# Kernel tuning notes

Measured on AMD Instinct MI355X. Metric: run time of the kernel, lower is better.

Reference implementation:

```python
import jax, jax.numpy as jnp
import numpy as np

B, S, D = 64, 256, 512          # batch, seq_len_max, num_dim (= in_dim = nclass)
H, DO = 8, 64                   # num_heads, out_dim per head (H*DO == D)
ALPHA = 0.2                     # leaky_relu negative slope
N = B * S                       # nodes
DEG = 32
E = N * DEG + N                 # random edges + self-loops


def setup_inputs() -> dict:
    key = jax.random.key(0)
    k = jax.random.split(key, 7)
    h = jax.random.normal(k[0], (B, S, D), jnp.float32)
    loops = jnp.arange(N, dtype=jnp.int32)
    src = jnp.concatenate([jax.random.randint(k[1], (N * DEG,), 0, N, jnp.int32), loops])
    dst = jnp.concatenate([jax.random.randint(k[2], (N * DEG,), 0, N, jnp.int32), loops])
    W1 = jax.random.normal(k[3], (H, D, DO), jnp.float32) * 0.05      # per-head fc weight
    a1 = jax.random.normal(k[4], (H, 2 * DO), jnp.float32) * 0.05     # per-head attn_fc weight
    Wout = jax.random.normal(k[5], (H * DO, D), jnp.float32) * 0.05   # out_att fc
    aout = jax.random.normal(k[6], (2 * D,), jnp.float32) * 0.05      # out_att attn_fc
    return {"h": h, "W1": W1, "a1": a1, "Wout": Wout, "aout": aout, "src": src, "dst": dst}


def gat_head(x, W, a, src, dst, concat):
    # x: [N, in_d], W: [in_d, d], a: [2d]
    z = x @ W                                   # [N, d]
    d = W.shape[1]
    es = z @ a[:d]                              # src part of attn score, [N]
    ed = z @ a[d:]                              # dst part, [N]
    e = jax.nn.leaky_relu(es[src] + ed[dst], ALPHA)   # [E]
    # segment softmax over incoming edges of each dst node
    m = jax.ops.segment_max(e, dst, num_segments=N)
    m = jnp.where(jnp.isfinite(m), m, 0.0)
    ex = jnp.exp(e - m[dst])
    den = jax.ops.segment_sum(ex, dst, num_segments=N)
    att = ex / den[dst]                         # [E] (self-loops guarantee den > 0)
    out = jax.ops.segment_sum(att[:, None] * z[src], dst, num_segments=N)  # [N, d]
    return jax.nn.elu(out) if concat else out


def reference(h, W1, a1, Wout, aout, src, dst):
    x = h.reshape(N, D)                         # dropout is identity at eval
    heads = jax.vmap(lambda W, a: gat_head(x, W, a, src, dst, True))(W1, a1)  # [H, N, DO]
    hcat = jnp.transpose(heads, (1, 0, 2)).reshape(N, H * DO)                 # [N, H*DO]
    out = jax.nn.elu(gat_head(hcat, Wout, aout, src, dst, False))             # [N, D]
    return (out + x).reshape(B, S, D)
```

## Files before the change

### kernel.cpp

```cpp
#include <hip/hip_runtime.h>
#include <stdint.h>

#define DD 512
#define HH 8
#define DOO 64
#define ALPHA 0.2f

typedef __attribute__((ext_vector_type(8))) short short8;
typedef __attribute__((ext_vector_type(4))) float floatx4;
typedef __attribute__((ext_vector_type(4))) unsigned short u16x4;
typedef unsigned short u16;

static __device__ __forceinline__ float bf2f(u16 u){
  union { unsigned int u; float f; } c; c.u = ((unsigned int)u) << 16; return c.f;
}
static __device__ __forceinline__ u16 f2bf(float f){
  union { float f; unsigned int u; } c; c.f = f;
  unsigned int u = c.u;
  unsigned int r = (u + 0x7FFFu + ((u >> 16) & 1u)) >> 16;
  return (u16)r;
}
static __device__ __forceinline__ float leaky(float s){ return (s >= 0.f) ? s : ALPHA * s; }
static __device__ __forceinline__ float elu(float v){ return (v > 0.f) ? v : (__expf(v) - 1.f); }

#define PERM_LO 0x01000504u
#define PERM_HI 0x03020706u

#define DOT2(accv, pairv, wv) \
  asm("v_dot2_f32_bf16 %0, %1, %2, %0" : "+v"(accv) : "v"(pairv), "v"(wv))

#define GLOAD_LDS16(g, l) \
  __builtin_amdgcn_global_load_lds((const __attribute__((address_space(1))) void*)(g), \
                                   (__attribute__((address_space(3))) void*)(l), 16, 0, 0)

__global__ void k_prep(const float* __restrict__ h, u16* __restrict__ xb,
                       const float* __restrict__ W1, u16* __restrict__ wbt1,
                       const float* __restrict__ Wout, u16* __restrict__ wbt2,
                       const int* __restrict__ dst, int* deg,
                       int n4, int E){
  int i = blockIdx.x * blockDim.x + threadIdx.x;
  if (i < n4){
    float4 v = ((const float4*)h)[i];
    u16x4 o;
    o[0] = f2bf(v.x); o[1] = f2bf(v.y); o[2] = f2bf(v.z); o[3] = f2bf(v.w);
    ((u16x4*)xb)[i] = o;
    return;
  }
  i -= n4;
  if (i < HH * DD * DOO / 8){
    int idx0 = i * 8;
    #pragma unroll
    for (int t = 0; t < 8; t++){
      int idx = idx0 + t;
      int hh = idx >> 15;
      int rem = idx & 32767;
      int k = rem >> 6;
      int dd = rem & 63;
      wbt1[(hh * 64 + dd) * DD + k] = f2bf(W1[idx]);
    }
    return;
  }
  i -= HH * DD * DOO / 8;
  if (i < DD * DD){
    int k = i >> 9, n = i & 511;
    wbt2[n * DD + k] = f2bf(Wout[i]);
    return;
  }
  i -= DD * DD;
  if (i < E) atomicAdd(&deg[dst[i]], 1);
}

__global__ void k_scan(const int* __restrict__ deg, int* __restrict__ off, int N){
  __shared__ int sm[1024];
  int tid = threadIdx.x;
  const int per = 16;
  int base = tid * per;
  int loc[per];
  int t = 0;
  #pragma unroll
  for (int i = 0; i < per; i++){
    int v = (base + i < N) ? deg[base + i] : 0;
    v = (v + 3) & ~3;
    loc[i] = v; t += v;
  }
  sm[tid] = t; __syncthreads();
  for (int o = 1; o < 1024; o <<= 1){
    int v = 0;
    if (tid >= o) v = sm[tid - o];
    __syncthreads();
    sm[tid] += v;
    __syncthreads();
  }
  int run = sm[tid] - t;
  #pragma unroll
  for (int i = 0; i < per; i++){ if (base + i < N) off[base + i] = run; run += loc[i]; }
  if (tid == 1023) off[N] = run;
}

__global__ void k_scatter(const int* __restrict__ src, const int* __restrict__ dst,
                          const int* __restrict__ off, int* cursor, int* __restrict__ csr,
                          int E, int N){
  int i = blockIdx.x * blockDim.x + threadIdx.x;
  if (i < 256){
    csr[off[N] + i] = 0;
  }
  if (i < E){
    int d = dst[i];
    int p = atomicAdd(&cursor[d], 1);
    csr[off[d] + p] = src[i];
  }
}

__global__ __launch_bounds__(256) void k_gemm(const u16* __restrict__ A,
                                              const u16* __restrict__ BT,
                                              u16* __restrict__ C, int M){
  __shared__ __attribute__((aligned(16))) u16 As[128 * 64];
  __shared__ __attribute__((aligned(16))) u16 Bs[128 * 64];
  const int tid = threadIdx.x;
  const int wid = tid >> 6, lane = tid & 63;
  const int n0 = blockIdx.x * 128, m0 = blockIdx.y * 128;
  const int wr = wid >> 1, wc = wid & 1;
  const int row16 = lane & 15, kg = lane >> 4;
  floatx4 acc[4][4];
  #pragma unroll
  for (int i = 0; i < 4; i++)
    #pragma unroll
    for (int j = 0; j < 4; j++) acc[i][j] = (floatx4)0.0f;

  for (int kt = 0; kt < DD; kt += 64){
    #pragma unroll
    for (int i = 0; i < 4; i++){
      int chunk = i * 256 + tid;
      int m = chunk >> 3, g = chunk & 7;
      int gs = g ^ (m & 7);
      GLOAD_LDS16(A + (size_t)(m0 + m) * DD + kt + gs * 8, &As[chunk * 8]);
      GLOAD_LDS16(BT + (size_t)(n0 + m) * DD + kt + gs * 8, &Bs[chunk * 8]);
    }
    __syncthreads();
    short8 af[4][2], bf[4][2];
    #pragma unroll
    for (int mi = 0; mi < 4; mi++)
      #pragma unroll
      for (int kk = 0; kk < 2; kk++){
        int row = wr * 64 + mi * 16 + row16;
        int gr = (kk * 4 + kg) ^ (row & 7);
        af[mi][kk] = *(const short8*)(&As[(row * 8 + gr) * 8]);
      }
    #pragma unroll
    for (int ni = 0; ni < 4; ni++)
      #pragma unroll
      for (int kk = 0; kk < 2; kk++){
        int row = wc * 64 + ni * 16 + row16;
        int gr = (kk * 4 + kg) ^ (row & 7);
        bf[ni][kk] = *(const short8*)(&Bs[(row * 8 + gr) * 8]);
      }
    #pragma unroll
    for (int kk = 0; kk < 2; kk++)
      #pragma unroll
      for (int mi = 0; mi < 4; mi++)
        #pragma unroll
        for (int ni = 0; ni < 4; ni++)
          acc[mi][ni] = __builtin_amdgcn_mfma_f32_16x16x32_bf16(af[mi][kk], bf[ni][kk], acc[mi][ni], 0, 0, 0);
    __syncthreads();
  }
  #pragma unroll
  for (int mi = 0; mi < 4; mi++)
    #pragma unroll
    for (int ni = 0; ni < 4; ni++)
      #pragma unroll
      for (int j = 0; j < 4; j++){
        int r = m0 + wr * 64 + mi * 16 + kg * 4 + j;
        int c = n0 + wc * 64 + ni * 16 + row16;
        C[(size_t)r * DD + c] = f2bf(acc[mi][ni][j]);
      }
}

__global__ void k_scores1(const u16* __restrict__ z, const float* __restrict__ a1,
                          float* __restrict__ es, float* __restrict__ ed, int N){
  int wid = threadIdx.x >> 6, lane = threadIdx.x & 63;
  int n = blockIdx.x * 4 + wid;
  if (n >= N) return;
  int h = lane >> 3, j8 = lane & 7;
  short8 zv = *(const short8*)(z + (size_t)n * DD + lane * 8);
  float esv = 0.f, edv = 0.f;
  #pragma unroll
  for (int t = 0; t < 8; t++){
    float f = bf2f((u16)zv[t]);
    esv += f * a1[h * 128 + j8 * 8 + t];
    edv += f * a1[h * 128 + 64 + j8 * 8 + t];
  }
  #pragma unroll
  for (int d2 = 1; d2 < 8; d2 <<= 1){ esv += __shfl_xor(esv, d2); edv += __shfl_xor(edv, d2); }
  if (j8 == 0){ es[n * 8 + h] = esv; ed[n * 8 + h] = edv; }
}

__global__ void k_scores2(const u16* __restrict__ z, const float* __restrict__ aout,
                          float* __restrict__ es, float* __restrict__ ed, int N){
  int wid = threadIdx.x >> 6, lane = threadIdx.x & 63;
  int n = blockIdx.x * 4 + wid;
  if (n >= N) return;
  short8 zv = *(const short8*)(z + (size_t)n * DD + lane * 8);
  float esv = 0.f, edv = 0.f;
  #pragma unroll
  for (int t = 0; t < 8; t++){
    float f = bf2f((u16)zv[t]);
    esv += f * aout[lane * 8 + t];
    edv += f * aout[512 + lane * 8 + t];
  }
  #pragma unroll
  for (int d2 = 1; d2 < 64; d2 <<= 1){ esv += __shfl_xor(esv, d2); edv += __shfl_xor(edv, d2); }
  if (lane == 0){ es[n] = esv; ed[n] = edv; }
}

__global__ void k_edgew1(const float* __restrict__ es, const float* __restrict__ ed,
                         const int* __restrict__ off, const int* __restrict__ deg,
                         int* __restrict__ csr, unsigned* __restrict__ wp,
                         float* __restrict__ den1, int N, int ep2){
  int wid = threadIdx.x >> 6, lane = threadIdx.x & 63;
  int n = blockIdx.x * 4 + wid;
  if (n >= N) return;
  int o0 = off[n], cntp = off[n + 1] - o0, cnt = deg[n];
  float edh[8];
  {
    float4 d0 = *(const float4*)(ed + (size_t)n * 8);
    float4 d1 = *(const float4*)(ed + (size_t)n * 8 + 4);
    edh[0]=d0.x; edh[1]=d0.y; edh[2]=d0.z; edh[3]=d0.w;
    edh[4]=d1.x; edh[5]=d1.y; edh[6]=d1.z; edh[7]=d1.w;
  }
  float den[8];
  #pragma unroll
  for (int h = 0; h < 8; h++) den[h] = 0.f;
  for (int base = 0; base < cntp; base += 64){
    int e = base + lane;
    float wv[8];
    if (e < cnt){
      int s = csr[o0 + e];
      float4 e0 = *(const float4*)(es + (size_t)s * 8);
      float4 e1 = *(const float4*)(es + (size_t)s * 8 + 4);
      float ev[8] = {e0.x, e0.y, e0.z, e0.w, e1.x, e1.y, e1.z, e1.w};
      #pragma unroll
      for (int h = 0; h < 8; h++){
        float w = __expf(leaky(ev[h] + edh[h]));
        wv[h] = w; den[h] += w;
      }
    } else {
      if (e < cntp) csr[o0 + e] = 0;
      #pragma unroll
      for (int h = 0; h < 8; h++) wv[h] = 0.f;
    }
    #pragma unroll
    for (int h = 0; h < 8; h++){
      float wn = __shfl_down(wv[h], 1);
      if (!(lane & 1) && e < cntp){
        unsigned pk;
        asm("v_cvt_pk_bf16_f32 %0, %1, %2" : "=v"(pk) : "v"(wv[h]), "v"(wn));
        wp[(size_t)h * ep2 + ((o0 + e) >> 1)] = pk;
      }
    }
  }
  #pragma unroll
  for (int h = 0; h < 8; h++){
    float d = den[h];
    #pragma unroll
    for (int d2 = 1; d2 < 64; d2 <<= 1) d += __shfl_xor(d, d2);
    if (lane == 0) den1[(size_t)n * 8 + h] = d;
  }
}

__global__ void k_edgew2(const float* __restrict__ es, const float* __restrict__ ed,
                         const int* __restrict__ off, const int* __restrict__ deg,
                         int* __restrict__ csr, unsigned* __restrict__ wp,
                         float* __restrict__ den2, int N){
  int wid = threadIdx.x >> 6, lane = threadIdx.x & 63;
  int n = blockIdx.x * 4 + wid;
  if (n >= N) return;
  int o0 = off[n], cntp = off[n + 1] - o0, cnt = deg[n];
  float edn = ed[n];
  float dsum = 0.f;
  for (int base = 0; base < cntp; base += 64){
    int e = base + lane;
    float w = 0.f;
    if (e < cnt){
      int s = csr[o0 + e];
      w = __expf(leaky(es[s] + edn));
      dsum += w;
    } else if (e < cntp){
      csr[o0 + e] = 0;
    }
    float wn = __shfl_down(w, 1);
    if (!(lane & 1) && e < cntp){
      unsigned pk;
      asm("v_cvt_pk_bf16_f32 %0, %1, %2" : "=v"(pk) : "v"(w), "v"(wn));
      wp[(o0 + e) >> 1] = pk;
    }
  }
  #pragma unroll
  for (int d2 = 1; d2 < 64; d2 <<= 1) dsum += __shfl_xor(dsum, d2);
  if (lane == 0) den2[n] = dsum;
}

__global__ __launch_bounds__(256) void k_agg1(const u16* __restrict__ z,
    const unsigned* __restrict__ wp, const float* __restrict__ den1,
    const int* __restrict__ off, const int* __restrict__ csr,
    u16* __restrict__ hcat, int N, int ep2){
  int wid = __builtin_amdgcn_readfirstlane(threadIdx.x >> 6);
  int lane = threadIdx.x & 63;
  int n = blockIdx.x * 4 + wid;
  if (n >= N) return;
  int p = blockIdx.y;
  int o0 = off[n];
  int itn = (off[n + 1] - o0) >> 2;
  const int4* cp4 = (const int4*)(csr + o0);
  const unsigned* zd = (const unsigned*)z + (size_t)p * 64 + lane;
  int head = 2 * p + (lane >> 5);
  const unsigned* wpb = wp + (size_t)head * ep2 + (o0 >> 1);
  float acc0 = 0.f, acc1 = 0.f;

  int4 c0 = cp4[0], c1 = cp4[1];
  uint2 a0 = *(const uint2*)(wpb);
  uint2 a1 = *(const uint2*)(wpb + 2);
  unsigned dA0 = zd[(size_t)(unsigned)c0.x * 256], dA1 = zd[(size_t)(unsigned)c0.y * 256];
  unsigned dB0 = zd[(size_t)(unsigned)c0.z * 256], dB1 = zd[(size_t)(unsigned)c0.w * 256];
  unsigned eA0 = zd[(size_t)(unsigned)c1.x * 256], eA1 = zd[(size_t)(unsigned)c1.y * 256];
  unsigned eB0 = zd[(size_t)(unsigned)c1.z * 256], eB1 = zd[(size_t)(unsigned)c1.w * 256];

  for (int it = 0; it < itn; ++it){
    int4 cn = cp4[it + 2];
    uint2 an = *(const uint2*)(wpb + 2 * it + 4);
    unsigned nA0 = zd[(size_t)(unsigned)cn.x * 256], nA1 = zd[(size_t)(unsigned)cn.y * 256];
    unsigned nB0 = zd[(size_t)(unsigned)cn.z * 256], nB1 = zd[(size_t)(unsigned)cn.w * 256];
    unsigned pr;
    pr = __builtin_amdgcn_perm(dA0, dA1, PERM_LO); DOT2(acc0, pr, a0.x);
    pr = __builtin_amdgcn_perm(dA0, dA1, PERM_HI); DOT2(acc1, pr, a0.x);
    pr = __builtin_amdgcn_perm(dB0, dB1, PERM_LO); DOT2(acc0, pr, a0.y);
    pr = __builtin_amdgcn_perm(dB0, dB1, PERM_HI); DOT2(acc1, pr, a0.y);
    dA0 = eA0; dA1 = eA1; dB0 = eB0; dB1 = eB1; a0 = a1;
    eA0 = nA0; eA1 = nA1; eB0 = nB0; eB1 = nB1; a1 = an;
  }
  float inv = 1.f / den1[(size_t)n * 8 + head];
  unsigned od = (unsigned)f2bf(elu(acc0 * inv)) | ((unsigned)f2bf(elu(acc1 * inv)) << 16);
  ((unsigned*)(hcat + (size_t)n * DD))[p * 64 + lane] = od;
}

__global__ __launch_bounds__(256) void k_agg2(const u16* __restrict__ z,
    const unsigned* __restrict__ wp, const float* __restrict__ den2,
    const int* __restrict__ off, const int* __restrict__ csr,
    const u16* __restrict__ xb, float* __restrict__ out, int N){
  int wid = __builtin_amdgcn_readfirstlane(threadIdx.x >> 6);
  int lane = threadIdx.x & 63;
  int n = blockIdx.x * 4 + wid;
  if (n >= N) return;
  int p = blockIdx.y;
  int o0 = off[n];
  int itn = (off[n + 1] - o0) >> 2;
  const int4* cp4 = (const int4*)(csr + o0);
  const unsigned* zd = (const unsigned*)z + (size_t)p * 64 + lane;
  const unsigned* wpb = wp + (o0 >> 1);
  float acc0 = 0.f, acc1 = 0.f;

  int4 c0 = cp4[0], c1 = cp4[1];
  uint2 a0 = *(const uint2*)(wpb);
  uint2 a1 = *(const uint2*)(wpb + 2);
  unsigned dA0 = zd[(size_t)(unsigned)c0.x * 256], dA1 = zd[(size_t)(unsigned)c0.y * 256];
  unsigned dB0 = zd[(size_t)(unsigned)c0.z * 256], dB1 = zd[(size_t)(unsigned)c0.w * 256];
  unsigned eA0 = zd[(size_t)(unsigned)c1.x * 256], eA1 = zd[(size_t)(unsigned)c1.y * 256];
  unsigned eB0 = zd[(size_t)(unsigned)c1.z * 256], eB1 = zd[(size_t)(unsigned)c1.w * 256];

  for (int it = 0; it < itn; ++it){
    int4 cn = cp4[it + 2];
    uint2 an = *(const uint2*)(wpb + 2 * it + 4);
    unsigned nA0 = zd[(size_t)(unsigned)cn.x * 256], nA1 = zd[(size_t)(unsigned)cn.y * 256];
    unsigned nB0 = zd[(size_t)(unsigned)cn.z * 256], nB1 = zd[(size_t)(unsigned)cn.w * 256];
    unsigned pr;
    pr = __builtin_amdgcn_perm(dA0, dA1, PERM_LO); DOT2(acc0, pr, a0.x);
    pr = __builtin_amdgcn_perm(dA0, dA1, PERM_HI); DOT2(acc1, pr, a0.x);
    pr = __builtin_amdgcn_perm(dB0, dB1, PERM_LO); DOT2(acc0, pr, a0.y);
    pr = __builtin_amdgcn_perm(dB0, dB1, PERM_HI); DOT2(acc1, pr, a0.y);
    dA0 = eA0; dA1 = eA1; dB0 = eB0; dB1 = eB1; a0 = a1;
    eA0 = nA0; eA1 = nA1; eB0 = nB0; eB1 = nB1; a1 = an;
  }
  float inv = 1.f / den2[n];
  unsigned xv = ((const unsigned*)(xb + (size_t)n * DD))[p * 64 + lane];
  float2 o2;
  o2.x = elu(acc0 * inv) + bf2f((u16)(xv & 0xFFFFu));
  o2.y = elu(acc1 * inv) + bf2f((u16)(xv >> 16));
  *(float2*)(out + (size_t)n * DD + p * 128 + lane * 2) = o2;
}

extern "C" void kernel_launch(void* const* d_in, const int* in_sizes, int n_in,
                              void* d_out, int out_size, void* d_ws, size_t ws_size,
                              hipStream_t stream){
  const float* h   = (const float*)d_in[0];
  const float* W1  = (const float*)d_in[1];
  const float* a1  = (const float*)d_in[2];
  const float* Wout= (const float*)d_in[3];
  const float* aout= (const float*)d_in[4];
  const int* src   = (const int*)d_in[5];
  const int* dst   = (const int*)d_in[6];
  float* out = (float*)d_out;
  const int N = in_sizes[0] / DD;
  const int E = in_sizes[5];
  const int EP = E + 3 * N + 512;
  const int ep2 = EP >> 1;

  char* p = (char*)d_ws;
  auto alloc = [&](size_t bytes) -> char* {
    char* r = p;
    p += (bytes + 255) & ~(size_t)255;
    return r;
  };
  u16* xb    = (u16*)alloc((size_t)N * DD * 2);
  u16* z1b   = (u16*)alloc((size_t)N * DD * 2);
  u16* hcat  = (u16*)alloc((size_t)N * DD * 2);
  u16* wbt1  = (u16*)alloc((size_t)DD * DD * 2);
  u16* wbt2  = (u16*)alloc((size_t)DD * DD * 2);
  float* es1 = (float*)alloc((size_t)N * HH * 4);
  float* ed1 = (float*)alloc((size_t)N * HH * 4);
  float* es2 = (float*)alloc((size_t)N * 4);
  float* ed2 = (float*)alloc((size_t)N * 4);
  float* den1= (float*)alloc((size_t)N * HH * 4);
  float* den2= (float*)alloc((size_t)N * 4);
  int* deg   = (int*)alloc((size_t)N * 4);
  int* off   = (int*)alloc((size_t)(N + 1) * 4);
  int* cursor= (int*)alloc((size_t)N * 4);
  int* csr   = (int*)alloc((size_t)EP * 4);
  unsigned* wp1 = (unsigned*)alloc(((size_t)HH * ep2 + 64) * 4);
  unsigned* wp2 = (unsigned*)alloc(((size_t)ep2 + 64) * 4);

  hipMemsetAsync(deg, 0, (size_t)((char*)csr - (char*)deg), stream);

  int n4 = N * DD / 4;
  int prep_threads = n4 + HH * DD * DOO / 8 + DD * DD + E;
  k_prep<<<(prep_threads + 255) / 256, 256, 0, stream>>>(h, xb, W1, wbt1, Wout, wbt2, dst, deg, n4, E);
  k_scan<<<1, 1024, 0, stream>>>(deg, off, N);
  k_scatter<<<(E + 255) / 256, 256, 0, stream>>>(src, dst, off, cursor, csr, E, N);

  dim3 gg(DD / 128, N / 128);
  dim3 ga((N + 3) / 4, 4);
  dim3 gw((N + 3) / 4);

  k_gemm<<<gg, 256, 0, stream>>>(xb, wbt1, z1b, N);
  k_scores1<<<(N + 3) / 4, 256, 0, stream>>>(z1b, a1, es1, ed1, N);
  k_edgew1<<<gw, 256, 0, stream>>>(es1, ed1, off, deg, csr, wp1, den1, N, ep2);
  k_agg1<<<ga, 256, 0, stream>>>(z1b, wp1, den1, off, csr, hcat, N, ep2);

  k_gemm<<<gg, 256, 0, stream>>>(hcat, wbt2, z1b, N);
  k_scores2<<<(N + 3) / 4, 256, 0, stream>>>(z1b, aout, es2, ed2, N);
  k_edgew2<<<gw, 256, 0, stream>>>(es2, ed2, off, deg, csr, wp2, den2, N);
  k_agg2<<<ga, 256, 0, stream>>>(z1b, wp2, den2, off, csr, xb, out, N);
}
```

Before: 252.3 us.

## Remap aggregation to one column per lane with sentinel-padded CSR

The aggregation kernels now map each lane to a single 16-bit column of one 64-wide slice, using 8 slices per node instead of 4 slices with two columns per lane. This removes the per-edge perm work but doubles the number of blocks and gathers only 2 bytes per lane per edge. CSR padding now uses a sentinel index N that points to a zeroed extra row of z, and the cursor is initialised to the offsets, so the edge-weight kernels read csr without branching and no longer write to it. This adds the k_ntot and k_fillpad launches.

```diff
diff --git a/kernel.cpp b/kernel.cpp
--- a/kernel.cpp
+++ b/kernel.cpp
@@ -23,11 +23,11 @@
 static __device__ __forceinline__ float leaky(float s){ return (s >= 0.f) ? s : ALPHA * s; }
 static __device__ __forceinline__ float elu(float v){ return (v > 0.f) ? v : (__expf(v) - 1.f); }
 
-#define PERM_LO 0x01000504u
-#define PERM_HI 0x03020706u
-
 #define DOT2(accv, pairv, wv) \
   asm("v_dot2_f32_bf16 %0, %1, %2, %0" : "+v"(accv) : "v"(pairv), "v"(wv))
+
+#define PACK2(dst, lo, hi) \
+  asm("v_lshl_or_b32 %0, %1, 16, %2" : "=v"(dst) : "v"(hi), "v"(lo))
 
 #define GLOAD_LDS16(g, l) \
   __builtin_amdgcn_global_load_lds((const __attribute__((address_space(1))) void*)(g), \
@@ -36,8 +36,8 @@
 __global__ void k_prep(const float* __restrict__ h, u16* __restrict__ xb,
                        const float* __restrict__ W1, u16* __restrict__ wbt1,
                        const float* __restrict__ Wout, u16* __restrict__ wbt2,
-                       const int* __restrict__ dst, int* deg,
-                       int n4, int E){
+                       const int* __restrict__ dst, int* deg, u16* __restrict__ z1b,
+                       int n4, int E, int N){
   int i = blockIdx.x * blockDim.x + threadIdx.x;
   if (i < n4){
     float4 v = ((const float4*)h)[i];
@@ -67,10 +67,24 @@
     return;
   }
   i -= DD * DD;
-  if (i < E) atomicAdd(&deg[dst[i]], 1);
-}
-
-__global__ void k_scan(const int* __restrict__ deg, int* __restrict__ off, int N){
+  if (i < E){
+    atomicAdd(&deg[dst[i]], 1);
+    return;
+  }
+  i -= E;
+  if (i < DD / 4){
+    u16x4 zz; zz[0]=0; zz[1]=0; zz[2]=0; zz[3]=0;
+    ((u16x4*)(z1b + (size_t)N * DD))[i] = zz;
+  }
+}
+
+__global__ void k_ntot(const int* __restrict__ deg, int* __restrict__ ntot, int N){
+  int n = blockIdx.x * blockDim.x + threadIdx.x;
+  if (n < N) ntot[n] = (deg[n] + 3) & ~3;
+}
+
+__global__ void k_scan(const int* __restrict__ ntot, int* __restrict__ off,
+                       int* __restrict__ cursor, int N){
   __shared__ int sm[1024];
   int tid = threadIdx.x;
   const int per = 16;
@@ -78,11 +92,7 @@
   int loc[per];
   int t = 0;
   #pragma unroll
-  for (int i = 0; i < per; i++){
-    int v = (base + i < N) ? deg[base + i] : 0;
-    v = (v + 3) & ~3;
-    loc[i] = v; t += v;
-  }
+  for (int i = 0; i < per; i++){ int v = (base + i < N) ? ntot[base + i] : 0; loc[i] = v; t += v; }
   sm[tid] = t; __syncthreads();
   for (int o = 1; o < 1024; o <<= 1){
     int v = 0;
@@ -93,7 +103,10 @@
   }
   int run = sm[tid] - t;
   #pragma unroll
-  for (int i = 0; i < per; i++){ if (base + i < N) off[base + i] = run; run += loc[i]; }
+  for (int i = 0; i < per; i++){
+    if (base + i < N){ off[base + i] = run; cursor[base + i] = run; }
+    run += loc[i];
+  }
   if (tid == 1023) off[N] = run;
 }
 
@@ -101,14 +114,22 @@
                           const int* __restrict__ off, int* cursor, int* __restrict__ csr,
                           int E, int N){
   int i = blockIdx.x * blockDim.x + threadIdx.x;
-  if (i < 256){
-    csr[off[N] + i] = 0;
+  if (i < 512){
+    csr[off[N] + i] = N;
   }
   if (i < E){
     int d = dst[i];
     int p = atomicAdd(&cursor[d], 1);
-    csr[off[d] + p] = src[i];
-  }
+    csr[p] = src[i];
+  }
+}
+
+__global__ void k_fillpad(const int* __restrict__ off, const int* __restrict__ cursor,
+                          int* __restrict__ csr, int N){
+  int n = blockIdx.x * blockDim.x + threadIdx.x;
+  if (n >= N) return;
+  int e = off[n + 1];
+  for (int q = cursor[n]; q < e; q++) csr[q] = N;
 }
 
 __global__ __launch_bounds__(256) void k_gemm(const u16* __restrict__ A,
@@ -213,13 +234,13 @@
 }
 
 __global__ void k_edgew1(const float* __restrict__ es, const float* __restrict__ ed,
-                         const int* __restrict__ off, const int* __restrict__ deg,
-                         int* __restrict__ csr, unsigned* __restrict__ wp,
+                         const int* __restrict__ off,
+                         const int* __restrict__ csr, unsigned* __restrict__ wp,
                          float* __restrict__ den1, int N, int ep2){
   int wid = threadIdx.x >> 6, lane = threadIdx.x & 63;
   int n = blockIdx.x * 4 + wid;
   if (n >= N) return;
-  int o0 = off[n], cntp = off[n + 1] - o0, cnt = deg[n];
+  int o0 = off[n], cntp = off[n + 1] - o0;
   float edh[8];
   {
     float4 d0 = *(const float4*)(ed + (size_t)n * 8);
@@ -232,21 +253,17 @@
   for (int h = 0; h < 8; h++) den[h] = 0.f;
   for (int base = 0; base < cntp; base += 64){
     int e = base + lane;
+    int s = csr[o0 + e];
+    bool valid = (e < cntp) && (s != N);
+    float4 e0 = *(const float4*)(es + (size_t)s * 8);
+    float4 e1 = *(const float4*)(es + (size_t)s * 8 + 4);
+    float ev[8] = {e0.x, e0.y, e0.z, e0.w, e1.x, e1.y, e1.z, e1.w};
     float wv[8];
-    if (e < cnt){
-      int s = csr[o0 + e];
-      float4 e0 = *(const float4*)(es + (size_t)s * 8);
-      float4 e1 = *(const float4*)(es + (size_t)s * 8 + 4);
-      float ev[8] = {e0.x, e0.y, e0.z, e0.w, e1.x, e1.y, e1.z, e1.w};
-      #pragma unroll
-      for (int h = 0; h < 8; h++){
-        float w = __expf(leaky(ev[h] + edh[h]));
-        wv[h] = w; den[h] += w;
-      }
-    } else {
-      if (e < cntp) csr[o0 + e] = 0;
-      #pragma unroll
-      for (int h = 0; h < 8; h++) wv[h] = 0.f;
+    #pragma unroll
+    for (int h = 0; h < 8; h++){
+      float w = __expf(leaky(ev[h] + edh[h]));
+      wv[h] = valid ? w : 0.f;
+      den[h] += wv[h];
     }
     #pragma unroll
     for (int h = 0; h < 8; h++){
@@ -268,25 +285,22 @@
 }
 
 __global__ void k_edgew2(const float* __restrict__ es, const float* __restrict__ ed,
-                         const int* __restrict__ off, const int* __restrict__ deg,
-                         int* __restrict__ csr, unsigned* __restrict__ wp,
+                         const int* __restrict__ off,
+                         const int* __restrict__ csr, unsigned* __restrict__ wp,
                          float* __restrict__ den2, int N){
   int wid = threadIdx.x >> 6, lane = threadIdx.x & 63;
   int n = blockIdx.x * 4 + wid;
   if (n >= N) return;
-  int o0 = off[n], cntp = off[n + 1] - o0, cnt = deg[n];
+  int o0 = off[n], cntp = off[n + 1] - o0;
   float edn = ed[n];
   float dsum = 0.f;
   for (int base = 0; base < cntp; base += 64){
     int e = base + lane;
-    float w = 0.f;
-    if (e < cnt){
-      int s = csr[o0 + e];
-      w = __expf(leaky(es[s] + edn));
-      dsum += w;
-    } else if (e < cntp){
-      csr[o0 + e] = 0;
-    }
+    int s = csr[o0 + e];
+    bool valid = (e < cntp) && (s != N);
+    float w = __expf(leaky(es[s] + edn));
+    w = valid ? w : 0.f;
+    dsum += w;
     float wn = __shfl_down(w, 1);
     if (!(lane & 1) && e < cntp){
       unsigned pk;
@@ -303,88 +317,92 @@
     const unsigned* __restrict__ wp, const float* __restrict__ den1,
     const int* __restrict__ off, const int* __restrict__ csr,
     u16* __restrict__ hcat, int N, int ep2){
-  int wid = __builtin_amdgcn_readfirstlane(threadIdx.x >> 6);
-  int lane = threadIdx.x & 63;
-  int n = blockIdx.x * 4 + wid;
-  if (n >= N) return;
-  int p = blockIdx.y;
+  int tid = threadIdx.x;
+  int wid = tid >> 6, lane = tid & 63;
+  int s = blockIdx.x & 7;
+  int n = (blockIdx.x >> 3) * 4 + wid;
+  if (n >= N) return;
   int o0 = off[n];
   int itn = (off[n + 1] - o0) >> 2;
   const int4* cp4 = (const int4*)(csr + o0);
-  const unsigned* zd = (const unsigned*)z + (size_t)p * 64 + lane;
-  int head = 2 * p + (lane >> 5);
-  const unsigned* wpb = wp + (size_t)head * ep2 + (o0 >> 1);
-  float acc0 = 0.f, acc1 = 0.f;
-
-  int4 c0 = cp4[0], c1 = cp4[1];
-  uint2 a0 = *(const uint2*)(wpb);
-  uint2 a1 = *(const uint2*)(wpb + 2);
-  unsigned dA0 = zd[(size_t)(unsigned)c0.x * 256], dA1 = zd[(size_t)(unsigned)c0.y * 256];
-  unsigned dB0 = zd[(size_t)(unsigned)c0.z * 256], dB1 = zd[(size_t)(unsigned)c0.w * 256];
-  unsigned eA0 = zd[(size_t)(unsigned)c1.x * 256], eA1 = zd[(size_t)(unsigned)c1.y * 256];
-  unsigned eB0 = zd[(size_t)(unsigned)c1.z * 256], eB1 = zd[(size_t)(unsigned)c1.w * 256];
-
+  const uint2* wpb = (const uint2*)(wp + (size_t)s * ep2 + (o0 >> 1));
+  const u16* zs = z + s * 64 + lane;
+  float acc = 0.f;
+
+  unsigned dA0, dA1, dB0, dB1, eA0, eA1, eB0, eB1;
+  uint2 aq0, aq1;
+  int4 c1;
+  {
+    int4 c0 = cp4[0];
+    c1 = cp4[1];
+    aq0 = wpb[0]; aq1 = wpb[1];
+    dA0 = zs[(size_t)(unsigned)c0.x * DD]; dA1 = zs[(size_t)(unsigned)c0.y * DD];
+    dB0 = zs[(size_t)(unsigned)c0.z * DD]; dB1 = zs[(size_t)(unsigned)c0.w * DD];
+    eA0 = zs[(size_t)(unsigned)c1.x * DD]; eA1 = zs[(size_t)(unsigned)c1.y * DD];
+    eB0 = zs[(size_t)(unsigned)c1.z * DD]; eB1 = zs[(size_t)(unsigned)c1.w * DD];
+  }
   for (int it = 0; it < itn; ++it){
     int4 cn = cp4[it + 2];
-    uint2 an = *(const uint2*)(wpb + 2 * it + 4);
-    unsigned nA0 = zd[(size_t)(unsigned)cn.x * 256], nA1 = zd[(size_t)(unsigned)cn.y * 256];
-    unsigned nB0 = zd[(size_t)(unsigned)cn.z * 256], nB1 = zd[(size_t)(unsigned)cn.w * 256];
-    unsigned pr;
-    pr = __builtin_amdgcn_perm(dA0, dA1, PERM_LO); DOT2(acc0, pr, a0.x);
-    pr = __builtin_amdgcn_perm(dA0, dA1, PERM_HI); DOT2(acc1, pr, a0.x);
-    pr = __builtin_amdgcn_perm(dB0, dB1, PERM_LO); DOT2(acc0, pr, a0.y);
-    pr = __builtin_amdgcn_perm(dB0, dB1, PERM_HI); DOT2(acc1, pr, a0.y);
-    dA0 = eA0; dA1 = eA1; dB0 = eB0; dB1 = eB1; a0 = a1;
-    eA0 = nA0; eA1 = nA1; eB0 = nB0; eB1 = nB1; a1 = an;
-  }
-  float inv = 1.f / den1[(size_t)n * 8 + head];
-  unsigned od = (unsigned)f2bf(elu(acc0 * inv)) | ((unsigned)f2bf(elu(acc1 * inv)) << 16);
-  ((unsigned*)(hcat + (size_t)n * DD))[p * 64 + lane] = od;
+    uint2 an = wpb[it + 2];
+    unsigned nA0 = zs[(size_t)(unsigned)cn.x * DD], nA1 = zs[(size_t)(unsigned)cn.y * DD];
+    unsigned nB0 = zs[(size_t)(unsigned)cn.z * DD], nB1 = zs[(size_t)(unsigned)cn.w * DD];
+    unsigned pA, pB;
+    PACK2(pA, dA0, dA1);
+    PACK2(pB, dB0, dB1);
+    DOT2(acc, pA, aq0.x);
+    DOT2(acc, pB, aq0.y);
+    dA0 = eA0; dA1 = eA1; dB0 = eB0; dB1 = eB1; aq0 = aq1;
+    eA0 = nA0; eA1 = nA1; eB0 = nB0; eB1 = nB1; aq1 = an;
+  }
+  float inv = 1.f / den1[(size_t)n * 8 + s];
+  hcat[(size_t)n * DD + s * 64 + lane] = f2bf(elu(acc * inv));
 }
 
 __global__ __launch_bounds__(256) void k_agg2(const u16* __restrict__ z,
     const unsigned* __restrict__ wp, const float* __restrict__ den2,
     const int* __restrict__ off, const int* __restrict__ csr,
     const u16* __restrict__ xb, float* __restrict__ out, int N){
-  int wid = __builtin_amdgcn_readfirstlane(threadIdx.x >> 6);
-  int lane = threadIdx.x & 63;
-  int n = blockIdx.x * 4 + wid;
-  if (n >= N) return;
-  int p = blockIdx.y;
+  int tid = threadIdx.x;
+  int wid = tid >> 6, lane = tid & 63;
+  int s = blockIdx.x & 7;
+  int n = (blockIdx.x >> 3) * 4 + wid;
+  if (n >= N) return;
   int o0 = off[n];
   int itn = (off[n + 1] - o0) >> 2;
   const int4* cp4 = (const int4*)(csr + o0);
-  const unsigned* zd = (const unsigned*)z + (size_t)p * 64 + lane;
-  const unsigned* wpb = wp + (o0 >> 1);
-  float acc0 = 0.f, acc1 = 0.f;
-
-  int4 c0 = cp4[0], c1 = cp4[1];
-  uint2 a0 = *(const uint2*)(wpb);
-  uint2 a1 = *(const uint2*)(wpb + 2);
-  unsigned dA0 = zd[(size_t)(unsigned)c0.x * 256], dA1 = zd[(size_t)(unsigned)c0.y * 256];
-  unsigned dB0 = zd[(size_t)(unsigned)c0.z * 256], dB1 = zd[(size_t)(unsigned)c0.w * 256];
-  unsigned eA0 = zd[(size_t)(unsigned)c1.x * 256], eA1 = zd[(size_t)(unsigned)c1.y * 256];
-  unsigned eB0 = zd[(size_t)(unsigned)c1.z * 256], eB1 = zd[(size_t)(unsigned)c1.w * 256];
-
+  const uint2* wpb = (const uint2*)(wp + (o0 >> 1));
+  const u16* zs = z + s * 64 + lane;
+  float acc = 0.f;
+
+  unsigned dA0, dA1, dB0, dB1, eA0, eA1, eB0, eB1;
+  uint2 aq0, aq1;
+  int4 c1;
+  {
+    int4 c0 = cp4[0];
+    c1 = cp4[1];
+    aq0 = wpb[0]; aq1 = wpb[1];
+    dA0 = zs[(size_t)(unsigned)c0.x * DD]; dA1 = zs[(size_t)(unsigned)c0.y * DD];
+    dB0 = zs[(size_t)(unsigned)c0.z * DD]; dB1 = zs[(size_t)(unsigned)c0.w * DD];
+    eA0 = zs[(size_t)(unsigned)c1.x * DD]; eA1 = zs[(size_t)(unsigned)c1.y * DD];
+    eB0 = zs[(size_t)(unsigned)c1.z * DD]; eB1 = zs[(size_t)(unsigned)c1.w * DD];
+  }
   for (int it = 0; it < itn; ++it){
     int4 cn = cp4[it + 2];
-    uint2 an = *(const uint2*)(wpb + 2 * it + 4);
-    unsigned nA0 = zd[(size_t)(unsigned)cn.x * 256], nA1 = zd[(size_t)(unsigned)cn.y * 256];
-    unsigned nB0 = zd[(size_t)(unsigned)cn.z * 256], nB1 = zd[(size_t)(unsigned)cn.w * 256];
-    unsigned pr;
-    pr = __builtin_amdgcn_perm(dA0, dA1, PERM_LO); DOT2(acc0, pr, a0.x);
-    pr = __builtin_amdgcn_perm(dA0, dA1, PERM_HI); DOT2(acc1, pr, a0.x);
-    pr = __builtin_amdgcn_perm(dB0, dB1, PERM_LO); DOT2(acc0, pr, a0.y);
-    pr = __builtin_amdgcn_perm(dB0, dB1, PERM_HI); DOT2(acc1, pr, a0.y);
-    dA0 = eA0; dA1 = eA1; dB0 = eB0; dB1 = eB1; a0 = a1;
-    eA0 = nA0; eA1 = nA1; eB0 = nB0; eB1 = nB1; a1 = an;
+    uint2 an = wpb[it + 2];
+    unsigned nA0 = zs[(size_t)(unsigned)cn.x * DD], nA1 = zs[(size_t)(unsigned)cn.y * DD];
+    unsigned nB0 = zs[(size_t)(unsigned)cn.z * DD], nB1 = zs[(size_t)(unsigned)cn.w * DD];
+    unsigned pA, pB;
+    PACK2(pA, dA0, dA1);
+    PACK2(pB, dB0, dB1);
+    DOT2(acc, pA, aq0.x);
+    DOT2(acc, pB, aq0.y);
+    dA0 = eA0; dA1 = eA1; dB0 = eB0; dB1 = eB1; aq0 = aq1;
+    eA0 = nA0; eA1 = nA1; eB0 = nB0; eB1 = nB1; aq1 = an;
   }
   float inv = 1.f / den2[n];
-  unsigned xv = ((const unsigned*)(xb + (size_t)n * DD))[p * 64 + lane];
-  float2 o2;
-  o2.x = elu(acc0 * inv) + bf2f((u16)(xv & 0xFFFFu));
-  o2.y = elu(acc1 * inv) + bf2f((u16)(xv >> 16));
-  *(float2*)(out + (size_t)n * DD + p * 128 + lane * 2) = o2;
+  int c = s * 64 + lane;
+  float xv = bf2f(xb[(size_t)n * DD + c]);
+  out[(size_t)n * DD + c] = elu(acc * inv) + xv;
 }
 
 extern "C" void kernel_launch(void* const* d_in, const int* in_sizes, int n_in,
@@ -410,42 +428,46 @@
     return r;
   };
   u16* xb    = (u16*)alloc((size_t)N * DD * 2);
-  u16* z1b   = (u16*)alloc((size_t)N * DD * 2);
+  u16* z1b   = (u16*)alloc((size_t)(N + 1) * DD * 2);
   u16* hcat  = (u16*)alloc((size_t)N * DD * 2);
   u16* wbt1  = (u16*)alloc((size_t)DD * DD * 2);
   u16* wbt2  = (u16*)alloc((size_t)DD * DD * 2);
-  float* es1 = (float*)alloc((size_t)N * HH * 4);
+  float* es1 = (float*)alloc(((size_t)N * HH + 8) * 4);
   float* ed1 = (float*)alloc((size_t)N * HH * 4);
-  float* es2 = (float*)alloc((size_t)N * 4);
+  float* es2 = (float*)alloc(((size_t)N + 8) * 4);
   float* ed2 = (float*)alloc((size_t)N * 4);
   float* den1= (float*)alloc((size_t)N * HH * 4);
   float* den2= (float*)alloc((size_t)N * 4);
   int* deg   = (int*)alloc((size_t)N * 4);
+  int* ntot  = (int*)alloc((size_t)N * 4);
   int* off   = (int*)alloc((size_t)(N + 1) * 4);
   int* cursor= (int*)alloc((size_t)N * 4);
   int* csr   = (int*)alloc((size_t)EP * 4);
   unsigned* wp1 = (unsigned*)alloc(((size_t)HH * ep2 + 64) * 4);
   unsigned* wp2 = (unsigned*)alloc(((size_t)ep2 + 64) * 4);
 
-  hipMemsetAsync(deg, 0, (size_t)((char*)csr - (char*)deg), stream);
+  hipMemsetAsync(deg, 0, (size_t)N * 4, stream);
 
   int n4 = N * DD / 4;
-  int prep_threads = n4 + HH * DD * DOO / 8 + DD * DD + E;
-  k_prep<<<(prep_threads + 255) / 256, 256, 0, stream>>>(h, xb, W1, wbt1, Wout, wbt2, dst, deg, n4, E);
-  k_scan<<<1, 1024, 0, stream>>>(deg, off, N);
+  int prep_threads = n4 + HH * DD * DOO / 8 + DD * DD + E + DD / 4;
+  k_prep<<<(prep_threads + 255) / 256, 256, 0, stream>>>(h, xb, W1, wbt1, Wout, wbt2,
+                                                         dst, deg, z1b, n4, E, N);
+  k_ntot<<<(N + 255) / 256, 256, 0, stream>>>(deg, ntot, N);
+  k_scan<<<1, 1024, 0, stream>>>(ntot, off, cursor, N);
   k_scatter<<<(E + 255) / 256, 256, 0, stream>>>(src, dst, off, cursor, csr, E, N);
+  k_fillpad<<<(N + 255) / 256, 256, 0, stream>>>(off, cursor, csr, N);
 
   dim3 gg(DD / 128, N / 128);
-  dim3 ga((N + 3) / 4, 4);
+  dim3 ga(8 * ((N + 3) / 4));
   dim3 gw((N + 3) / 4);
 
   k_gemm<<<gg, 256, 0, stream>>>(xb, wbt1, z1b, N);
   k_scores1<<<(N + 3) / 4, 256, 0, stream>>>(z1b, a1, es1, ed1, N);
-  k_edgew1<<<gw, 256, 0, stream>>>(es1, ed1, off, deg, csr, wp1, den1, N, ep2);
+  k_edgew1<<<gw, 256, 0, stream>>>(es1, ed1, off, csr, wp1, den1, N, ep2);
   k_agg1<<<ga, 256, 0, stream>>>(z1b, wp1, den1, off, csr, hcat, N, ep2);
 
   k_gemm<<<gg, 256, 0, stream>>>(hcat, wbt2, z1b, N);
   k_scores2<<<(N + 3) / 4, 256, 0, stream>>>(z1b, aout, es2, ed2, N);
-  k_edgew2<<<gw, 256, 0, stream>>>(es2, ed2, off, deg, csr, wp2, den2, N);
+  k_edgew2<<<gw, 256, 0, stream>>>(es2, ed2, off, csr, wp2, den2, N);
   k_agg2<<<ga, 256, 0, stream>>>(z1b, wp2, den2, off, csr, xb, out, N);
 }
```

Result: slower. 405.7 us (+60.8%).
